# Kernel optimization log

Measured on AMD Instinct MI355X. Metric: run time of the kernel, lower is better.

The kernel has to match this reference:

```python
import jax, jax.numpy as jnp
import numpy as np

N_NODES = 100000
N_EDGES = 1600000
IN_C, HID_C, OUT_C = 128, 128, 64


def setup_inputs() -> dict:
    key = jax.random.key(0)
    ks = jax.random.split(key, 5)
    x = jax.random.normal(ks[0], (N_NODES, IN_C), dtype=jnp.float32)
    edge_index = jax.random.randint(ks[1], (2, N_EDGES), 0, N_NODES, dtype=jnp.int32)
    W1 = jax.random.normal(ks[2], (IN_C, HID_C), dtype=jnp.float32) * (1.0 / np.sqrt(IN_C))
    W2 = jax.random.normal(ks[3], (HID_C, HID_C), dtype=jnp.float32) * (1.0 / np.sqrt(HID_C))
    W3 = jax.random.normal(ks[4], (HID_C, OUT_C), dtype=jnp.float32) * (1.0 / np.sqrt(HID_C))
    b1 = jnp.zeros((HID_C,), jnp.float32)
    b2 = jnp.zeros((HID_C,), jnp.float32)
    b3 = jnp.zeros((OUT_C,), jnp.float32)
    return {"x": x, "edge_index": edge_index, "W1": W1, "b1": b1,
            "W2": W2, "b2": b2, "W3": W3, "b3": b3}


def _gcn_norm(edge_index, num_nodes):
    # PyG gcn_norm: add self-loops, symmetric normalization D^-1/2 A D^-1/2
    loops = jnp.arange(num_nodes, dtype=edge_index.dtype)
    row = jnp.concatenate([edge_index[0], loops])  # source nodes
    col = jnp.concatenate([edge_index[1], loops])  # target nodes
    ones = jnp.ones(row.shape[0], jnp.float32)
    deg = jax.ops.segment_sum(ones, col, num_segments=num_nodes)
    dinv = jnp.where(deg > 0, jax.lax.rsqrt(deg), 0.0)
    norm = dinv[row] * dinv[col]  # [E + N]
    return row, col, norm


def _gcn_conv(h, row, col, norm, W, b, num_nodes):
    h = h @ W                                   # [N, out] dense transform first
    msg = h[row] * norm[:, None]                # gather + scale, [E+N, out]
    out = jax.ops.segment_sum(msg, col, num_segments=num_nodes)  # scatter-add
    return out + b


def reference(x, edge_index, W1, b1, W2, b2, W3, b3):
    n = x.shape[0]
    row, col, norm = _gcn_norm(edge_index, n)
    h = jax.nn.relu(_gcn_conv(x, row, col, norm, W1, b1, n))
    h = jax.nn.relu(_gcn_conv(h, row, col, norm, W2, b2, n))
    h = _gcn_conv(h, row, col, norm, W3, b3, n)
    return h
```

## Files before the change

### kernel.cpp

```cpp
#include <hip/hip_runtime.h>
#include <hip/hip_fp16.h>


#define K_DIM 128
#define CHUNK 8192
#define NBMAX 1024
#define BSH 8
#define BMASK 255

typedef _Float16 f16x8 __attribute__((ext_vector_type(8)));
typedef float f32x4 __attribute__((ext_vector_type(4)));


__global__ __launch_bounds__(256) void hist_pass(const int* __restrict__ col, int E,
                                                 int NB, int B1, int* __restrict__ histG) {
    __shared__ int h[NBMAX];
    const int tid = threadIdx.x;
    for (int i = tid; i < NB; i += 256) h[i] = 0;
    __syncthreads();
    const int base = blockIdx.x * CHUNK;
    const int end = min(base + CHUNK, E);
    for (int e = base + tid; e < end; e += 256) atomicAdd(&h[col[e] >> BSH], 1);
    __syncthreads();
    for (int i = tid; i < NB; i += 256) histG[(size_t)i * B1 + blockIdx.x] = h[i];
}

__global__ __launch_bounds__(256) void scan_blocks(int* __restrict__ data, int n,
                                                   int* __restrict__ bsum) {
    __shared__ int sh[256];
    const int tid = threadIdx.x;
    const int base = blockIdx.x * 1024;
    int v[4];
    int sum = 0;
#pragma unroll
    for (int j = 0; j < 4; ++j) {
        int i = base + tid * 4 + j;
        v[j] = (i < n) ? data[i] : 0;
        sum += v[j];
    }
    sh[tid] = sum;
    __syncthreads();
#pragma unroll
    for (int off = 1; off < 256; off <<= 1) {
        int t = (tid >= off) ? sh[tid - off] : 0;
        __syncthreads();
        sh[tid] += t;
        __syncthreads();
    }
    int run = (tid > 0) ? sh[tid - 1] : 0;
#pragma unroll
    for (int j = 0; j < 4; ++j) {
        int i = base + tid * 4 + j;
        if (i < n) data[i] = run;
        run += v[j];
    }
    if (tid == 255) bsum[blockIdx.x] = sh[255];
}

__global__ __launch_bounds__(256) void scan_single(int* __restrict__ data, int n) {
    __shared__ int sh[256];
    const int tid = threadIdx.x;
    int v[4];
    int sum = 0;
#pragma unroll
    for (int j = 0; j < 4; ++j) {
        int i = tid * 4 + j;
        v[j] = (i < n) ? data[i] : 0;
        sum += v[j];
    }
    sh[tid] = sum;
    __syncthreads();
#pragma unroll
    for (int off = 1; off < 256; off <<= 1) {
        int t = (tid >= off) ? sh[tid - off] : 0;
        __syncthreads();
        sh[tid] += t;
        __syncthreads();
    }
    int run = (tid > 0) ? sh[tid - 1] : 0;
#pragma unroll
    for (int j = 0; j < 4; ++j) {
        int i = tid * 4 + j;
        if (i < n) data[i] = run;
        run += v[j];
    }
}

__global__ __launch_bounds__(256) void scatter_pass(const int* __restrict__ row,
                                                    const int* __restrict__ col, int E,
                                                    int NB, int B1,
                                                    const int* __restrict__ histG,
                                                    const int* __restrict__ bsum,
                                                    int* __restrict__ ebuf) {
    __shared__ int cur[NBMAX];
    const int tid = threadIdx.x;
    for (int i = tid; i < NB; i += 256) {
        const size_t idx = (size_t)i * B1 + blockIdx.x;
        cur[i] = histG[idx] + bsum[idx >> 10];
    }
    __syncthreads();
    const int base = blockIdx.x * CHUNK;
    const int end = min(base + CHUNK, E);
    for (int e = base + tid; e < end; e += 256) {
        int d = col[e];
        int s = row[e];
        int pos = atomicAdd(&cur[d >> BSH], 1);
        ebuf[pos] = (s << BSH) | (d & BMASK);
    }
}

__global__ __launch_bounds__(256) void build_csr(const int* __restrict__ ebuf,
                                                 const int* __restrict__ histG,
                                                 const int* __restrict__ bsum,
                                                 int NB, int B1, int N, int E,
                                                 int* __restrict__ offs,
                                                 float* __restrict__ dinv,
                                                 int* __restrict__ csr) {
    __shared__ int cnt[256];
    __shared__ int scn[256];
    __shared__ int curL[256];
    const int tid = threadIdx.x;
    const int b = blockIdx.x;
    const size_t iS = (size_t)b * B1;
    const int S = histG[iS] + bsum[iS >> 10];
    int T = E;
    if (b + 1 < NB) {
        const size_t iT = (size_t)(b + 1) * B1;
        T = histG[iT] + bsum[iT >> 10];
    }

    cnt[tid] = 0;
    __syncthreads();
    for (int i = S + tid; i < T; i += 256) atomicAdd(&cnt[ebuf[i] & BMASK], 1);
    __syncthreads();
    scn[tid] = cnt[tid];
    __syncthreads();
#pragma unroll
    for (int off = 1; off < 256; off <<= 1) {
        int t = (tid >= off) ? scn[tid - off] : 0;
        __syncthreads();
        scn[tid] += t;
        __syncthreads();
    }
    {
        int exc = (tid > 0) ? scn[tid - 1] : 0;
        int node = b * 256 + tid;
        if (node < N) {
            offs[node] = S + exc;
            dinv[node] = rsqrtf((float)(cnt[tid] + 1));
        }
        curL[tid] = S + exc;
    }
    if (b == 0 && tid == 0) offs[N] = E;
    __syncthreads();
    for (int i = S + tid; i < T; i += 256) {
        int p = ebuf[i];
        int pos = atomicAdd(&curL[p & BMASK], 1);
        csr[pos] = p >> BSH;
    }
}

__global__ void prep_wT(const float* __restrict__ W1, const float* __restrict__ W2,
                        const float* __restrict__ W3, __half* __restrict__ wT1,
                        __half* __restrict__ wT2, __half* __restrict__ wT3) {
    int tid = blockIdx.x * 256 + threadIdx.x;
    if (tid < 16384) {
        int n = tid >> 7, k = tid & 127;
        wT1[tid] = __float2half(W1[k * 128 + n]);
    } else if (tid < 32768) {
        int t = tid - 16384;
        int n = t >> 7, k = t & 127;
        wT2[t] = __float2half(W2[k * 128 + n]);
    } else if (tid < 40960) {
        int t = tid - 32768;
        int n = t >> 7, k = t & 127;
        wT3[t] = __float2half(W3[k * 64 + n]);
    }
}


__global__ __launch_bounds__(256) void gemm_x(const float* __restrict__ X,
                                              const __half* __restrict__ wT,
                                              const float* __restrict__ dinv,
                                              __half* __restrict__ out, int M) {
    const int tid = threadIdx.x;
    const int wave = tid >> 6;
    const int l = tid & 63;
    const int lm = l & 15;
    const int kg = l >> 4;
    const int row0 = blockIdx.x * 128 + wave * 32;

    f32x4 acc[2][8];
#pragma unroll
    for (int mt = 0; mt < 2; ++mt)
#pragma unroll
        for (int nt = 0; nt < 8; ++nt) acc[mt][nt] = {0.f, 0.f, 0.f, 0.f};

    const int m0 = row0 + lm;
    const int m1 = row0 + 16 + lm;
    const int mc0 = min(m0, M - 1);
    const int mc1 = min(m1, M - 1);

#pragma unroll
    for (int ks = 0; ks < 4; ++ks) {
        const int k0 = ks * 32 + kg * 8;
        float4 u0 = *(const float4*)&X[(size_t)mc0 * 128 + k0];
        float4 u1 = *(const float4*)&X[(size_t)mc0 * 128 + k0 + 4];
        float4 u2 = *(const float4*)&X[(size_t)mc1 * 128 + k0];
        float4 u3 = *(const float4*)&X[(size_t)mc1 * 128 + k0 + 4];
        f16x8 b0 = {(_Float16)u0.x, (_Float16)u0.y, (_Float16)u0.z, (_Float16)u0.w,
                    (_Float16)u1.x, (_Float16)u1.y, (_Float16)u1.z, (_Float16)u1.w};
        f16x8 b1 = {(_Float16)u2.x, (_Float16)u2.y, (_Float16)u2.z, (_Float16)u2.w,
                    (_Float16)u3.x, (_Float16)u3.y, (_Float16)u3.z, (_Float16)u3.w};
#pragma unroll
        for (int nt = 0; nt < 8; ++nt) {
            f16x8 a = *(const f16x8*)&wT[(size_t)(nt * 16 + lm) * 128 + k0];
            acc[0][nt] = __builtin_amdgcn_mfma_f32_16x16x32_f16(a, b0, acc[0][nt], 0, 0, 0);
            acc[1][nt] = __builtin_amdgcn_mfma_f32_16x16x32_f16(a, b1, acc[1][nt], 0, 0, 0);
        }
    }

#pragma unroll
    for (int mt = 0; mt < 2; ++mt) {
        const int m = (mt == 0) ? m0 : m1;
        if (m < M) {
            const float dv = dinv[m];
#pragma unroll
            for (int nt = 0; nt < 8; ++nt) {
                float z0 = acc[mt][nt][0] * dv, z1 = acc[mt][nt][1] * dv;
                float z2 = acc[mt][nt][2] * dv, z3 = acc[mt][nt][3] * dv;
                __half2 o[2] = {__float22half2_rn(make_float2(z0, z1)),
                                __float22half2_rn(make_float2(z2, z3))};
                *(float2*)&out[(size_t)m * 128 + nt * 16 + kg * 4] = *(float2*)o;
            }
        }
    }
}


template <int NCOLS>
__global__ __launch_bounds__(256) void gemm_f16(const __half* __restrict__ A,
                                                const __half* __restrict__ wT,
                                                const float* __restrict__ dinv,
                                                __half* __restrict__ out, int M) {
    constexpr int NT = NCOLS / 16;
    __shared__ __half sWT[NCOLS][136];

    const int tid = threadIdx.x;
    for (int idx = tid; idx < NCOLS * 16; idx += 256) {
        int n = idx >> 4, kc = (idx & 15) * 8;
        *(float4*)&sWT[n][kc] = *(const float4*)&wT[n * 128 + kc];
    }
    __syncthreads();

    const int wave = tid >> 6;
    const int l = tid & 63;
    const int lm = l & 15;
    const int kg = l >> 4;
    const int row0 = blockIdx.x * 128 + wave * 32;

    f32x4 acc[2][NT];
#pragma unroll
    for (int mt = 0; mt < 2; ++mt)
#pragma unroll
        for (int nt = 0; nt < NT; ++nt) acc[mt][nt] = {0.f, 0.f, 0.f, 0.f};

    const int m0 = row0 + lm;
    const int m1 = row0 + 16 + lm;
    const int mc0 = min(m0, M - 1);
    const int mc1 = min(m1, M - 1);

#pragma unroll
    for (int ks = 0; ks < 4; ++ks) {
        const int k0 = ks * 32 + kg * 8;
        f16x8 b0 = *(const f16x8*)&A[(size_t)mc0 * 128 + k0];
        f16x8 b1 = *(const f16x8*)&A[(size_t)mc1 * 128 + k0];
#pragma unroll
        for (int nt = 0; nt < NT; ++nt) {
            f16x8 a = *(const f16x8*)&sWT[nt * 16 + lm][k0];
            acc[0][nt] = __builtin_amdgcn_mfma_f32_16x16x32_f16(a, b0, acc[0][nt], 0, 0, 0);
            acc[1][nt] = __builtin_amdgcn_mfma_f32_16x16x32_f16(a, b1, acc[1][nt], 0, 0, 0);
        }
    }

#pragma unroll
    for (int mt = 0; mt < 2; ++mt) {
        const int m = (mt == 0) ? m0 : m1;
        if (m < M) {
            const float dv = dinv[m];
#pragma unroll
            for (int nt = 0; nt < NT; ++nt) {
                float z0 = acc[mt][nt][0] * dv, z1 = acc[mt][nt][1] * dv;
                float z2 = acc[mt][nt][2] * dv, z3 = acc[mt][nt][3] * dv;
                __half2 o[2] = {__float22half2_rn(make_float2(z0, z1)),
                                __float22half2_rn(make_float2(z2, z3))};
                *(float2*)&out[(size_t)m * NCOLS + nt * 16 + kg * 4] = *(float2*)o;
            }
        }
    }
}


template <bool RELU>
__global__ __launch_bounds__(256) void agg128(const __half* __restrict__ h,
                                              const float* __restrict__ dinv,
                                              const int* __restrict__ offs,
                                              const int* __restrict__ csr,
                                              const float* __restrict__ bias,
                                              __half* __restrict__ out, int N) {
    const int wid = (blockIdx.x * 256 + threadIdx.x) >> 6;
    if (wid >= N) return;
    const int l = threadIdx.x & 63;
    const int q = l >> 4;
    const int c = l & 15;
    const int beg = offs[wid], end = offs[wid + 1];
    const float di = dinv[wid];
    const float4* __restrict__ hp = (const float4*)h;

    float a[8] = {0.f, 0.f, 0.f, 0.f, 0.f, 0.f, 0.f, 0.f};
    int e = beg;
    for (; e + 16 <= end; e += 16) {
        int s0 = csr[e + q];
        int s1 = csr[e + 4 + q];
        int s2 = csr[e + 8 + q];
        int s3 = csr[e + 12 + q];
        float4 r0 = hp[(size_t)s0 * 16 + c];
        float4 r1 = hp[(size_t)s1 * 16 + c];
        float4 r2 = hp[(size_t)s2 * 16 + c];
        float4 r3 = hp[(size_t)s3 * 16 + c];
        const __half* h0 = (const __half*)&r0;
        const __half* h1 = (const __half*)&r1;
        const __half* h2 = (const __half*)&r2;
        const __half* h3 = (const __half*)&r3;
#pragma unroll
        for (int j = 0; j < 8; ++j) a[j] += __half2float(h0[j]);
#pragma unroll
        for (int j = 0; j < 8; ++j) a[j] += __half2float(h1[j]);
#pragma unroll
        for (int j = 0; j < 8; ++j) a[j] += __half2float(h2[j]);
#pragma unroll
        for (int j = 0; j < 8; ++j) a[j] += __half2float(h3[j]);
    }
    for (; e < end; e += 8) {
        const int last = end - 1;
        int i0 = e + q, i1 = e + 4 + q;
        float m0 = (i0 < end) ? 1.f : 0.f;
        float m1 = (i1 < end) ? 1.f : 0.f;
        int s0 = csr[min(i0, last)];
        int s1 = csr[min(i1, last)];
        float4 r0 = hp[(size_t)s0 * 16 + c];
        float4 r1 = hp[(size_t)s1 * 16 + c];
        const __half* h0 = (const __half*)&r0;
        const __half* h1 = (const __half*)&r1;
#pragma unroll
        for (int j = 0; j < 8; ++j) a[j] = fmaf(__half2float(h0[j]), m0, a[j]);
#pragma unroll
        for (int j = 0; j < 8; ++j) a[j] = fmaf(__half2float(h1[j]), m1, a[j]);
    }
#pragma unroll
    for (int j = 0; j < 8; ++j) {
        a[j] += __shfl_xor(a[j], 16);
        a[j] += __shfl_xor(a[j], 32);
    }
    {
        float4 rs = hp[(size_t)wid * 16 + c];
        const __half* hs = (const __half*)&rs;
#pragma unroll
        for (int j = 0; j < 8; ++j) a[j] += __half2float(hs[j]);
    }
    float4 b0 = ((const float4*)bias)[2 * c];
    float4 b1 = ((const float4*)bias)[2 * c + 1];
    float z[8];
    z[0] = fmaf(di, a[0], b0.x); z[1] = fmaf(di, a[1], b0.y);
    z[2] = fmaf(di, a[2], b0.z); z[3] = fmaf(di, a[3], b0.w);
    z[4] = fmaf(di, a[4], b1.x); z[5] = fmaf(di, a[5], b1.y);
    z[6] = fmaf(di, a[6], b1.z); z[7] = fmaf(di, a[7], b1.w);
    if (RELU) {
#pragma unroll
        for (int j = 0; j < 8; ++j) z[j] = fmaxf(z[j], 0.f);
    }
    if (q == 0) {
        __half2 o[4] = {__float22half2_rn(make_float2(z[0], z[1])),
                        __float22half2_rn(make_float2(z[2], z[3])),
                        __float22half2_rn(make_float2(z[4], z[5])),
                        __float22half2_rn(make_float2(z[6], z[7]))};
        ((float4*)out)[(size_t)wid * 16 + c] = *(float4*)o;
    }
}

__global__ __launch_bounds__(256) void agg64(const __half* __restrict__ h,
                                             const float* __restrict__ dinv,
                                             const int* __restrict__ offs,
                                             const int* __restrict__ csr,
                                             const float* __restrict__ bias,
                                             float* __restrict__ out, int N) {
    const int wid = (blockIdx.x * 256 + threadIdx.x) >> 6;
    if (wid >= N) return;
    const int l = threadIdx.x & 63;
    const int q = l >> 3;
    const int c = l & 7;
    const int beg = offs[wid], end = offs[wid + 1];
    const float di = dinv[wid];
    const float4* __restrict__ hp = (const float4*)h;

    float a[8] = {0.f, 0.f, 0.f, 0.f, 0.f, 0.f, 0.f, 0.f};
    int e = beg;
    for (; e + 16 <= end; e += 16) {
        int s0 = csr[e + q];
        int s1 = csr[e + 8 + q];
        float4 r0 = hp[(size_t)s0 * 8 + c];
        float4 r1 = hp[(size_t)s1 * 8 + c];
        const __half* h0 = (const __half*)&r0;
        const __half* h1 = (const __half*)&r1;
#pragma unroll
        for (int j = 0; j < 8; ++j) a[j] += __half2float(h0[j]);
#pragma unroll
        for (int j = 0; j < 8; ++j) a[j] += __half2float(h1[j]);
    }
    for (; e < end; e += 8) {
        const int last = end - 1;
        int i0 = e + q;
        float m0 = (i0 < end) ? 1.f : 0.f;
        int s0 = csr[min(i0, last)];
        float4 r0 = hp[(size_t)s0 * 8 + c];
        const __half* h0 = (const __half*)&r0;
#pragma unroll
        for (int j = 0; j < 8; ++j) a[j] = fmaf(__half2float(h0[j]), m0, a[j]);
    }
#pragma unroll
    for (int j = 0; j < 8; ++j) {
        a[j] += __shfl_xor(a[j], 8);
        a[j] += __shfl_xor(a[j], 16);
        a[j] += __shfl_xor(a[j], 32);
    }
    {
        float4 rs = hp[(size_t)wid * 8 + c];
        const __half* hs = (const __half*)&rs;
#pragma unroll
        for (int j = 0; j < 8; ++j) a[j] += __half2float(hs[j]);
    }
    float4 b0 = ((const float4*)bias)[2 * c];
    float4 b1 = ((const float4*)bias)[2 * c + 1];
    float z[8];
    z[0] = fmaf(di, a[0], b0.x); z[1] = fmaf(di, a[1], b0.y);
    z[2] = fmaf(di, a[2], b0.z); z[3] = fmaf(di, a[3], b0.w);
    z[4] = fmaf(di, a[4], b1.x); z[5] = fmaf(di, a[5], b1.y);
    z[6] = fmaf(di, a[6], b1.z); z[7] = fmaf(di, a[7], b1.w);
    if (q == 0) {
        ((float4*)out)[(size_t)wid * 16 + 2 * c] = make_float4(z[0], z[1], z[2], z[3]);
        ((float4*)out)[(size_t)wid * 16 + 2 * c + 1] = make_float4(z[4], z[5], z[6], z[7]);
    }
}


extern "C" void kernel_launch(void* const* d_in, const int* in_sizes, int n_in,
                              void* d_out, int out_size, void* d_ws, size_t ws_size,
                              hipStream_t stream) {
    const float* x  = (const float*)d_in[0];
    const int*   ei = (const int*)d_in[1];
    const float* W1 = (const float*)d_in[2];
    const float* b1 = (const float*)d_in[3];
    const float* W2 = (const float*)d_in[4];
    const float* b2 = (const float*)d_in[5];
    const float* W3 = (const float*)d_in[6];
    const float* b3 = (const float*)d_in[7];

    const int N = in_sizes[0] / 128;
    const int E = in_sizes[1] / 2;
    const int* row = ei;
    const int* col = ei + E;

    const int NB = (N + BMASK) >> BSH;
    const int B1 = (E + CHUNK - 1) / CHUNK;
    const int NBB1 = NB * B1;

    char* p = (char*)d_ws;
    auto alloc = [&](size_t bytes) {
        char* r = p;
        p += (bytes + 255) & ~(size_t)255;
        return r;
    };
    int*    offs  = (int*)alloc((size_t)(N + 1) * 4);
    float*  dinv  = (float*)alloc((size_t)N * 4);
    int*    histG = (int*)alloc((size_t)NBB1 * 4);
    int*    bsum  = (int*)alloc(1024 * 4);
    int*    ebuf  = (int*)alloc((size_t)E * 4);
    int*    csr   = (int*)alloc((size_t)E * 4);
    __half* bufA  = (__half*)alloc((size_t)N * 128 * 2);
    __half* bufB  = (__half*)alloc((size_t)N * 128 * 2);
    __half* wT1   = (__half*)alloc(16384 * 2);
    __half* wT2   = (__half*)alloc(16384 * 2);
    __half* wT3   = (__half*)alloc(8192 * 2);

    const int nsb = (NBB1 + 1023) / 1024;

    hist_pass<<<B1, 256, 0, stream>>>(col, E, NB, B1, histG);
    scan_blocks<<<nsb, 256, 0, stream>>>(histG, NBB1, bsum);
    scan_single<<<1, 256, 0, stream>>>(bsum, nsb);
    scatter_pass<<<B1, 256, 0, stream>>>(row, col, E, NB, B1, histG, bsum, ebuf);
    build_csr<<<NB, 256, 0, stream>>>(ebuf, histG, bsum, NB, B1, N, E, offs, dinv, csr);

    prep_wT<<<160, 256, 0, stream>>>(W1, W2, W3, wT1, wT2, wT3);

    const int gTile = (N + 127) / 128;
    const int gAgg = (N + 3) / 4;

    gemm_x<<<gTile, 256, 0, stream>>>(x, wT1, dinv, bufA, N);
    agg128<true><<<gAgg, 256, 0, stream>>>(bufA, dinv, offs, csr, b1, bufB, N);

    gemm_f16<128><<<gTile, 256, 0, stream>>>(bufB, wT2, dinv, bufA, N);
    agg128<true><<<gAgg, 256, 0, stream>>>(bufA, dinv, offs, csr, b2, bufB, N);

    gemm_f16<64><<<gTile, 256, 0, stream>>>(bufB, wT3, dinv, bufA, N);
    agg64<<<gAgg, 256, 0, stream>>>(bufA, dinv, offs, csr, b3, (float*)d_out, N);
}
```

Baseline: 280.0 us.

## Vectorize CSR build loops, add nontemporal loads/stores, drop LDS weight staging

The histogram and scatter passes now read edge indices as int4 vectors, and the chunk size is halved so more blocks are launched. Nontemporal loads and stores are added for the streamed inputs, CSR indices and aggregation outputs, to keep the gathered feature rows in cache. The f16 GEMM no longer stages transposed weights in shared memory and reads them directly from global memory. Together these aim to lower memory traffic and overhead, but the smaller chunk enlarges the histogram and scan work, and the direct weight reads depend on cache hits.

```diff
diff --git a/kernel.cpp b/kernel.cpp
--- a/kernel.cpp
+++ b/kernel.cpp
@@ -3,7 +3,7 @@
 
 
 #define K_DIM 128
-#define CHUNK 8192
+#define CHUNK 4096
 #define NBMAX 1024
 #define BSH 8
 #define BMASK 255
@@ -19,8 +19,19 @@
     for (int i = tid; i < NB; i += 256) h[i] = 0;
     __syncthreads();
     const int base = blockIdx.x * CHUNK;
-    const int end = min(base + CHUNK, E);
-    for (int e = base + tid; e < end; e += 256) atomicAdd(&h[col[e] >> BSH], 1);
+    const int bend = min(base + CHUNK, E);
+    for (int idx = base + tid * 4; idx < bend; idx += 1024) {
+        if (idx + 4 <= bend) {
+            int4 c4 = *(const int4*)&col[idx];
+            atomicAdd(&h[c4.x >> BSH], 1);
+            atomicAdd(&h[c4.y >> BSH], 1);
+            atomicAdd(&h[c4.z >> BSH], 1);
+            atomicAdd(&h[c4.w >> BSH], 1);
+        } else {
+            for (int j = 0; j < 4 && idx + j < bend; ++j)
+                atomicAdd(&h[col[idx + j] >> BSH], 1);
+        }
+    }
     __syncthreads();
     for (int i = tid; i < NB; i += 256) histG[(size_t)i * B1 + blockIdx.x] = h[i];
 }
@@ -100,12 +111,27 @@
     }
     __syncthreads();
     const int base = blockIdx.x * CHUNK;
-    const int end = min(base + CHUNK, E);
-    for (int e = base + tid; e < end; e += 256) {
-        int d = col[e];
-        int s = row[e];
-        int pos = atomicAdd(&cur[d >> BSH], 1);
-        ebuf[pos] = (s << BSH) | (d & BMASK);
+    const int bend = min(base + CHUNK, E);
+    for (int idx = base + tid * 4; idx < bend; idx += 1024) {
+        if (idx + 4 <= bend) {
+            int4 d4 = *(const int4*)&col[idx];
+            int4 s4 = *(const int4*)&row[idx];
+            int p0 = atomicAdd(&cur[d4.x >> BSH], 1);
+            ebuf[p0] = (s4.x << BSH) | (d4.x & BMASK);
+            int p1 = atomicAdd(&cur[d4.y >> BSH], 1);
+            ebuf[p1] = (s4.y << BSH) | (d4.y & BMASK);
+            int p2 = atomicAdd(&cur[d4.z >> BSH], 1);
+            ebuf[p2] = (s4.z << BSH) | (d4.z & BMASK);
+            int p3 = atomicAdd(&cur[d4.w >> BSH], 1);
+            ebuf[p3] = (s4.w << BSH) | (d4.w & BMASK);
+        } else {
+            for (int j = 0; j < 4 && idx + j < bend; ++j) {
+                int d = col[idx + j];
+                int s = row[idx + j];
+                int pos = atomicAdd(&cur[d >> BSH], 1);
+                ebuf[pos] = (s << BSH) | (d & BMASK);
+            }
+        }
     }
 }
 
@@ -204,10 +230,10 @@
 #pragma unroll
     for (int ks = 0; ks < 4; ++ks) {
         const int k0 = ks * 32 + kg * 8;
-        float4 u0 = *(const float4*)&X[(size_t)mc0 * 128 + k0];
-        float4 u1 = *(const float4*)&X[(size_t)mc0 * 128 + k0 + 4];
-        float4 u2 = *(const float4*)&X[(size_t)mc1 * 128 + k0];
-        float4 u3 = *(const float4*)&X[(size_t)mc1 * 128 + k0 + 4];
+        f32x4 u0 = __builtin_nontemporal_load((const f32x4*)&X[(size_t)mc0 * 128 + k0]);
+        f32x4 u1 = __builtin_nontemporal_load((const f32x4*)&X[(size_t)mc0 * 128 + k0 + 4]);
+        f32x4 u2 = __builtin_nontemporal_load((const f32x4*)&X[(size_t)mc1 * 128 + k0]);
+        f32x4 u3 = __builtin_nontemporal_load((const f32x4*)&X[(size_t)mc1 * 128 + k0 + 4]);
         f16x8 b0 = {(_Float16)u0.x, (_Float16)u0.y, (_Float16)u0.z, (_Float16)u0.w,
                     (_Float16)u1.x, (_Float16)u1.y, (_Float16)u1.z, (_Float16)u1.w};
         f16x8 b1 = {(_Float16)u2.x, (_Float16)u2.y, (_Float16)u2.z, (_Float16)u2.w,
@@ -244,15 +270,7 @@
                                                 const float* __restrict__ dinv,
                                                 __half* __restrict__ out, int M) {
     constexpr int NT = NCOLS / 16;
-    __shared__ __half sWT[NCOLS][136];
-
-    const int tid = threadIdx.x;
-    for (int idx = tid; idx < NCOLS * 16; idx += 256) {
-        int n = idx >> 4, kc = (idx & 15) * 8;
-        *(float4*)&sWT[n][kc] = *(const float4*)&wT[n * 128 + kc];
-    }
-    __syncthreads();
-
+    const int tid = threadIdx.x;
     const int wave = tid >> 6;
     const int l = tid & 63;
     const int lm = l & 15;
@@ -273,11 +291,11 @@
 #pragma unroll
     for (int ks = 0; ks < 4; ++ks) {
         const int k0 = ks * 32 + kg * 8;
-        f16x8 b0 = *(const f16x8*)&A[(size_t)mc0 * 128 + k0];
-        f16x8 b1 = *(const f16x8*)&A[(size_t)mc1 * 128 + k0];
+        f16x8 b0 = __builtin_nontemporal_load((const f16x8*)&A[(size_t)mc0 * 128 + k0]);
+        f16x8 b1 = __builtin_nontemporal_load((const f16x8*)&A[(size_t)mc1 * 128 + k0]);
 #pragma unroll
         for (int nt = 0; nt < NT; ++nt) {
-            f16x8 a = *(const f16x8*)&sWT[nt * 16 + lm][k0];
+            f16x8 a = *(const f16x8*)&wT[(size_t)(nt * 16 + lm) * 128 + k0];
             acc[0][nt] = __builtin_amdgcn_mfma_f32_16x16x32_f16(a, b0, acc[0][nt], 0, 0, 0);
             acc[1][nt] = __builtin_amdgcn_mfma_f32_16x16x32_f16(a, b1, acc[1][nt], 0, 0, 0);
         }
@@ -315,19 +333,19 @@
     const int c = l & 15;
     const int beg = offs[wid], end = offs[wid + 1];
     const float di = dinv[wid];
-    const float4* __restrict__ hp = (const float4*)h;
+    const f32x4* __restrict__ hp = (const f32x4*)h;
 
     float a[8] = {0.f, 0.f, 0.f, 0.f, 0.f, 0.f, 0.f, 0.f};
     int e = beg;
     for (; e + 16 <= end; e += 16) {
-        int s0 = csr[e + q];
-        int s1 = csr[e + 4 + q];
-        int s2 = csr[e + 8 + q];
-        int s3 = csr[e + 12 + q];
-        float4 r0 = hp[(size_t)s0 * 16 + c];
-        float4 r1 = hp[(size_t)s1 * 16 + c];
-        float4 r2 = hp[(size_t)s2 * 16 + c];
-        float4 r3 = hp[(size_t)s3 * 16 + c];
+        int s0 = __builtin_nontemporal_load(&csr[e + q]);
+        int s1 = __builtin_nontemporal_load(&csr[e + 4 + q]);
+        int s2 = __builtin_nontemporal_load(&csr[e + 8 + q]);
+        int s3 = __builtin_nontemporal_load(&csr[e + 12 + q]);
+        f32x4 r0 = hp[(size_t)s0 * 16 + c];
+        f32x4 r1 = hp[(size_t)s1 * 16 + c];
+        f32x4 r2 = hp[(size_t)s2 * 16 + c];
+        f32x4 r3 = hp[(size_t)s3 * 16 + c];
         const __half* h0 = (const __half*)&r0;
         const __half* h1 = (const __half*)&r1;
         const __half* h2 = (const __half*)&r2;
@@ -348,8 +366,8 @@
         float m1 = (i1 < end) ? 1.f : 0.f;
         int s0 = csr[min(i0, last)];
         int s1 = csr[min(i1, last)];
-        float4 r0 = hp[(size_t)s0 * 16 + c];
-        float4 r1 = hp[(size_t)s1 * 16 + c];
+        f32x4 r0 = hp[(size_t)s0 * 16 + c];
+        f32x4 r1 = hp[(size_t)s1 * 16 + c];
         const __half* h0 = (const __half*)&r0;
         const __half* h1 = (const __half*)&r1;
 #pragma unroll
@@ -363,7 +381,7 @@
         a[j] += __shfl_xor(a[j], 32);
     }
     {
-        float4 rs = hp[(size_t)wid * 16 + c];
+        f32x4 rs = hp[(size_t)wid * 16 + c];
         const __half* hs = (const __half*)&rs;
 #pragma unroll
         for (int j = 0; j < 8; ++j) a[j] += __half2float(hs[j]);
@@ -384,7 +402,7 @@
                         __float22half2_rn(make_float2(z[2], z[3])),
                         __float22half2_rn(make_float2(z[4], z[5])),
                         __float22half2_rn(make_float2(z[6], z[7]))};
-        ((float4*)out)[(size_t)wid * 16 + c] = *(float4*)o;
+        __builtin_nontemporal_store(*(f32x4*)o, (f32x4*)out + (size_t)wid * 16 + c);
     }
 }
 
@@ -401,15 +419,15 @@
     const int c = l & 7;
     const int beg = offs[wid], end = offs[wid + 1];
     const float di = dinv[wid];
-    const float4* __restrict__ hp = (const float4*)h;
+    const f32x4* __restrict__ hp = (const f32x4*)h;
 
     float a[8] = {0.f, 0.f, 0.f, 0.f, 0.f, 0.f, 0.f, 0.f};
     int e = beg;
     for (; e + 16 <= end; e += 16) {
-        int s0 = csr[e + q];
-        int s1 = csr[e + 8 + q];
-        float4 r0 = hp[(size_t)s0 * 8 + c];
-        float4 r1 = hp[(size_t)s1 * 8 + c];
+        int s0 = __builtin_nontemporal_load(&csr[e + q]);
+        int s1 = __builtin_nontemporal_load(&csr[e + 8 + q]);
+        f32x4 r0 = hp[(size_t)s0 * 8 + c];
+        f32x4 r1 = hp[(size_t)s1 * 8 + c];
         const __half* h0 = (const __half*)&r0;
         const __half* h1 = (const __half*)&r1;
 #pragma unroll
@@ -422,7 +440,7 @@
         int i0 = e + q;
         float m0 = (i0 < end) ? 1.f : 0.f;
         int s0 = csr[min(i0, last)];
-        float4 r0 = hp[(size_t)s0 * 8 + c];
+        f32x4 r0 = hp[(size_t)s0 * 8 + c];
         const __half* h0 = (const __half*)&r0;
 #pragma unroll
         for (int j = 0; j < 8; ++j) a[j] = fmaf(__half2float(h0[j]), m0, a[j]);
@@ -434,21 +452,20 @@
         a[j] += __shfl_xor(a[j], 32);
     }
     {
-        float4 rs = hp[(size_t)wid * 8 + c];
+        f32x4 rs = hp[(size_t)wid * 8 + c];
         const __half* hs = (const __half*)&rs;
 #pragma unroll
         for (int j = 0; j < 8; ++j) a[j] += __half2float(hs[j]);
     }
     float4 b0 = ((const float4*)bias)[2 * c];
     float4 b1 = ((const float4*)bias)[2 * c + 1];
-    float z[8];
-    z[0] = fmaf(di, a[0], b0.x); z[1] = fmaf(di, a[1], b0.y);
-    z[2] = fmaf(di, a[2], b0.z); z[3] = fmaf(di, a[3], b0.w);
-    z[4] = fmaf(di, a[4], b1.x); z[5] = fmaf(di, a[5], b1.y);
-    z[6] = fmaf(di, a[6], b1.z); z[7] = fmaf(di, a[7], b1.w);
+    f32x4 z0v = {fmaf(di, a[0], b0.x), fmaf(di, a[1], b0.y),
+                 fmaf(di, a[2], b0.z), fmaf(di, a[3], b0.w)};
+    f32x4 z1v = {fmaf(di, a[4], b1.x), fmaf(di, a[5], b1.y),
+                 fmaf(di, a[6], b1.z), fmaf(di, a[7], b1.w)};
     if (q == 0) {
-        ((float4*)out)[(size_t)wid * 16 + 2 * c] = make_float4(z[0], z[1], z[2], z[3]);
-        ((float4*)out)[(size_t)wid * 16 + 2 * c + 1] = make_float4(z[4], z[5], z[6], z[7]);
+        __builtin_nontemporal_store(z0v, (f32x4*)out + (size_t)wid * 16 + 2 * c);
+        __builtin_nontemporal_store(z1v, (f32x4*)out + (size_t)wid * 16 + 2 * c + 1);
     }
 }
 
```

Measured after the change: 301.2 us. +7.6%, slower.
